# Kernel optimization log

Hardware: AMD Instinct MI355X
Metric: run time of the kernel (lower is better)

The kernel has to match this reference:

```python
import jax, jax.numpy as jnp
import numpy as np

N_NODES = 50000
N_EDGES = 800000
IN_CH = 128
HID = 128


def _linear_params(key, fan_in, fan_out):
    kw, kb = jax.random.split(key)
    bound = 1.0 / np.sqrt(fan_in)
    W = jax.random.uniform(kw, (fan_in, fan_out), jnp.float32, -bound, bound)
    b = jax.random.uniform(kb, (fan_out,), jnp.float32, -bound, bound)
    return W, b


def setup_inputs() -> dict:
    key = jax.random.key(0)
    ks = jax.random.split(key, 11)
    x = jax.random.normal(ks[0], (N_NODES, IN_CH), jnp.float32)
    guidance_features = jax.random.normal(ks[1], (N_NODES, HID), jnp.float32)
    edge_index = jax.random.randint(ks[2], (2, N_EDGES), 0, N_NODES, jnp.int64)
    node_W, node_b = _linear_params(ks[3], IN_CH, HID)
    nbr_W, nbr_b = _linear_params(ks[4], IN_CH, HID)
    gud_W, gud_b = _linear_params(ks[5], HID, HID)
    enc_W, enc_b = _linear_params(ks[6], 3 * HID, HID)
    vp_W1, vp_b1 = _linear_params(ks[7], HID, HID // 2)
    vp_W2, vp_b2 = _linear_params(ks[8], HID // 2, 1)
    pol_W1, pol_b1 = _linear_params(ks[9], HID, HID)
    pol_W2, pol_b2 = _linear_params(ks[10], HID, 1)
    return dict(x=x, edge_index=edge_index, guidance_features=guidance_features,
                node_W=node_W, node_b=node_b, nbr_W=nbr_W, nbr_b=nbr_b,
                gud_W=gud_W, gud_b=gud_b, enc_W=enc_W, enc_b=enc_b,
                vp_W1=vp_W1, vp_b1=vp_b1, vp_W2=vp_W2, vp_b2=vp_b2,
                pol_W1=pol_W1, pol_b1=pol_b1, pol_W2=pol_W2, pol_b2=pol_b2)


def reference(x, edge_index, guidance_features,
              node_W, node_b, nbr_W, nbr_b, gud_W, gud_b,
              enc_W, enc_b, vp_W1, vp_b1, vp_W2, vp_b2,
              pol_W1, pol_b1, pol_W2, pol_b2):
    row, col = edge_index[0], edge_index[1]
    # Edge-wise gathers feeding three linear transforms -> [E, 3*HID] state
    node_feat = x[row] @ node_W + node_b            # [E, HID]
    nbr_feat = x[col] @ nbr_W + nbr_b               # [E, HID]
    gud_feat = guidance_features[col] @ gud_W + gud_b  # [E, HID]
    state = jnp.concatenate([node_feat, nbr_feat, gud_feat], axis=1)
    # state_encoder (eval mode: dropout = identity)
    enc = jax.nn.relu(state @ enc_W + enc_b)        # [E, HID]
    # value_predictor
    value_preds = jax.nn.relu(enc @ vp_W1 + vp_b1) @ vp_W2 + vp_b2  # [E, 1]
    # policy_net
    action_probs = jax.nn.sigmoid(
        jax.nn.relu(enc @ pol_W1 + pol_b1) @ pol_W2 + pol_b2)      # [E, 1]
    actions = (action_probs > 0.5).astype(x.dtype)  # eval-mode actions
    value_loss = jnp.zeros((), x.dtype)             # eval mode, labels=None
    return value_preds, action_probs, actions, value_loss
```

## Files before the change

kernel.cpp:

```cpp
#include <hip/hip_runtime.h>
#include <math.h>

#define N_NODES 50000
#define N_EDGES 800000

typedef __attribute__((ext_vector_type(8))) short short8_t;
typedef __attribute__((ext_vector_type(4))) float float4_t;

union U8 { short8_t v; unsigned short u[8]; };

__device__ __forceinline__ unsigned short bf16_rn(float f) {
    unsigned u = __float_as_uint(f);
    u += 0x7fffu + ((u >> 16) & 1u);
    return (unsigned short)(u >> 16);
}
__device__ __forceinline__ float bf2f(unsigned short h) {
    return __uint_as_float((unsigned)h << 16);
}
__device__ __forceinline__ void split3(float f, unsigned short& s0,
                                       unsigned short& s1, unsigned short& s2) {
    s0 = bf16_rn(f);  float r = f - bf2f(s0);
    s1 = bf16_rn(r);  r -= bf2f(s1);
    s2 = bf16_rn(r);
}


__global__ __launch_bounds__(256) void prep_kernel(
    const float* __restrict__ node_W, const float* __restrict__ node_b,
    const float* __restrict__ nbr_W,  const float* __restrict__ nbr_b,
    const float* __restrict__ gud_W,  const float* __restrict__ gud_b,
    const float* __restrict__ enc_W,  const float* __restrict__ enc_b,
    const float* __restrict__ vp_W1,  const float* __restrict__ vp_b1,
    const float* __restrict__ vp_W2,  const float* __restrict__ pol_W1,
    const float* __restrict__ pol_b1, const float* __restrict__ pol_W2,
    unsigned short* __restrict__ BTn0, unsigned short* __restrict__ BTn1,
    unsigned short* __restrict__ BTn2,
    unsigned short* __restrict__ BTg0, unsigned short* __restrict__ BTg1,
    unsigned short* __restrict__ BTg2,
    unsigned short* __restrict__ BTw0, unsigned short* __restrict__ BTw1,
    unsigned short* __restrict__ BTw2,
    float* __restrict__ cb, float* __restrict__ b1c, float* __restrict__ W2c,
    int* __restrict__ flags)
{
    const int k = blockIdx.x;
    const int j = threadIdx.x;
    if (j < 128) {
        float a = 0.f, b = 0.f;
        #pragma unroll 4
        for (int m = 0; m < 128; ++m) {
            a = fmaf(node_W[k * 128 + m], enc_W[m * 128 + j], a);
            b = fmaf(gud_W [k * 128 + m], enc_W[(256 + m) * 128 + j], b);
        }
        size_t i1 = (size_t)j * 128 + k;
        split3(a, BTn0[i1], BTn1[i1], BTn2[i1]);
        split3(b, BTg0[i1], BTg1[i1], BTg2[i1]);
    } else {
        const int n = j - 128;
        float a = 0.f;
        #pragma unroll 4
        for (int m = 0; m < 128; ++m)
            a = fmaf(nbr_W[k * 128 + m], enc_W[(128 + m) * 128 + n], a);
        size_t i2 = (size_t)(128 + n) * 128 + k;
        split3(a, BTn0[i2], BTn1[i2], BTn2[i2]);
    }
    if (j < 192) {
        float wv = (j < 64) ? vp_W1[k * 64 + j] : pol_W1[k * 128 + (j - 64)];
        size_t iw = (size_t)j * 128 + k;
        split3(wv, BTw0[iw], BTw1[iw], BTw2[iw]);
    }
    if (k == 0) {
        if (j < 128) {
            float cc = enc_b[j];
            for (int m = 0; m < 128; ++m) {
                cc = fmaf(node_b[m], enc_W[m * 128 + j], cc);
                cc = fmaf(nbr_b [m], enc_W[(128 + m) * 128 + j], cc);
                cc = fmaf(gud_b [m], enc_W[(256 + m) * 128 + j], cc);
            }
            cb[j] = cc;
        }
        if (j < 192) {
            b1c[j] = (j < 64) ? vp_b1[j] : pol_b1[j - 64];
            W2c[j] = (j < 64) ? vp_W2[j] : pol_W2[j - 64];
        }
        if (j < 64) {
            const int l = j, li = l & 15, lq = l >> 4;
            U8 A, B;
            #pragma unroll
            for (int u = 0; u < 8; ++u) { A.u[u] = 0; B.u[u] = 0; }
            if (lq == 0) {
                A.u[0] = bf16_rn((float)(li + 1));
                A.u[1] = bf16_rn(1.0f);
                B.u[0] = bf16_rn(1.0f);
                B.u[1] = bf16_rn((float)(100 * (li + 1)));
            }
            float4_t d = (float4_t){0.f, 0.f, 0.f, 0.f};
            d = __builtin_amdgcn_mfma_f32_16x16x32_bf16(A.v, B.v, d, 0, 0, 0);
            if (l == 17) {
                flags[0] = (fabsf(d[2] - 702.f) < 1.0f) ? 1 : 0;
            }
        }
    }
}

__global__ __launch_bounds__(256, 2) void node_kernel(
    const float* __restrict__ x, const float* __restrict__ g,
    const unsigned short* __restrict__ BTn0, const unsigned short* __restrict__ BTn1,
    const unsigned short* __restrict__ BTn2,
    const unsigned short* __restrict__ BTg0, const unsigned short* __restrict__ BTg1,
    const unsigned short* __restrict__ BTg2,
    const float* __restrict__ cb, const int* __restrict__ flags,
    float* __restrict__ P, float* __restrict__ Q)
{
    const int t = threadIdx.x;
    const int w = t >> 6, lane = t & 63;
    const int i16 = lane & 15, q = lane >> 4;
    const int base = blockIdx.x * 64;
    const bool qhalf = (w >= 2);
    const int nt0 = w * 4;
    const int kcmax = qhalf ? 8 : 4;
    const int swap = flags[0];

    float4_t acc[4][4];
    #pragma unroll
    for (int mt = 0; mt < 4; ++mt)
        #pragma unroll
        for (int nt = 0; nt < 4; ++nt) acc[mt][nt] = (float4_t){0.f, 0.f, 0.f, 0.f};

    for (int kc = 0; kc < kcmax; ++kc) {
        short8_t b0[4], b1v[4], b2v[4];
        #pragma unroll
        for (int nt = 0; nt < 4; ++nt) {
            if (kc < 4) {
                size_t roff = ((size_t)((nt0 + nt) * 16 + i16)) * 128 + kc * 32 + q * 8;
                b0[nt]  = *(const short8_t*)(BTn0 + roff);
                b1v[nt] = *(const short8_t*)(BTn1 + roff);
                b2v[nt] = *(const short8_t*)(BTn2 + roff);
            } else {
                size_t roff = ((size_t)((nt0 + nt - 8) * 16 + i16)) * 128 + (kc - 4) * 32 + q * 8;
                b0[nt]  = *(const short8_t*)(BTg0 + roff);
                b1v[nt] = *(const short8_t*)(BTg1 + roff);
                b2v[nt] = *(const short8_t*)(BTg2 + roff);
            }
        }
        #pragma unroll
        for (int mt = 0; mt < 4; ++mt) {
            int node = base + mt * 16 + i16; if (node > N_NODES - 1) node = N_NODES - 1;
            const float* src = (kc < 4)
                ? (x + (size_t)node * 128 + kc * 32 + q * 8)
                : (g + (size_t)node * 128 + (kc - 4) * 32 + q * 8);
            float4 v0 = *(const float4*)(src);
            float4 v1 = *(const float4*)(src + 4);
            float e[8] = {v0.x, v0.y, v0.z, v0.w, v1.x, v1.y, v1.z, v1.w};
            U8 a0, a1, a2;
            #pragma unroll
            for (int u = 0; u < 8; ++u) split3(e[u], a0.u[u], a1.u[u], a2.u[u]);
            #pragma unroll
            for (int nt = 0; nt < 4; ++nt) {
                float4_t c = acc[mt][nt];
                c = __builtin_amdgcn_mfma_f32_16x16x32_bf16(a0.v, b0[nt],  c, 0, 0, 0);
                c = __builtin_amdgcn_mfma_f32_16x16x32_bf16(a0.v, b1v[nt], c, 0, 0, 0);
                c = __builtin_amdgcn_mfma_f32_16x16x32_bf16(a1.v, b0[nt],  c, 0, 0, 0);
                c = __builtin_amdgcn_mfma_f32_16x16x32_bf16(a0.v, b2v[nt], c, 0, 0, 0);
                c = __builtin_amdgcn_mfma_f32_16x16x32_bf16(a1.v, b1v[nt], c, 0, 0, 0);
                c = __builtin_amdgcn_mfma_f32_16x16x32_bf16(a2.v, b0[nt],  c, 0, 0, 0);
                acc[mt][nt] = c;
            }
        }
    }

    if (!swap) {
        #pragma unroll
        for (int mt = 0; mt < 4; ++mt)
            #pragma unroll
            for (int nt = 0; nt < 4; ++nt) {
                int chan = (nt0 + nt) * 16 + i16;
                float bias = qhalf ? 0.f : cb[chan];
                #pragma unroll
                for (int r = 0; r < 4; ++r) {
                    int node = base + mt * 16 + q * 4 + r;
                    if (node < N_NODES) {
                        if (!qhalf) P[(size_t)node * 128 + chan] = acc[mt][nt][r] + bias;
                        else        Q[(size_t)node * 128 + (chan - 128)] = acc[mt][nt][r];
                    }
                }
            }
    } else {
        #pragma unroll
        for (int mt = 0; mt < 4; ++mt) {
            int node = base + mt * 16 + i16;
            if (node < N_NODES) {
                #pragma unroll
                for (int nt = 0; nt < 4; ++nt) {
                    int chanb = (nt0 + nt) * 16 + q * 4;
                    float4 vv;
                    vv.x = acc[mt][nt][0] + (!qhalf ? cb[chanb + 0] : 0.f);
                    vv.y = acc[mt][nt][1] + (!qhalf ? cb[chanb + 1] : 0.f);
                    vv.z = acc[mt][nt][2] + (!qhalf ? cb[chanb + 2] : 0.f);
                    vv.w = acc[mt][nt][3] + (!qhalf ? cb[chanb + 3] : 0.f);
                    if (!qhalf) *(float4*)(P + (size_t)node * 128 + chanb) = vv;
                    else        *(float4*)(Q + (size_t)node * 128 + chanb - 128) = vv;
                }
            }
        }
    }
}

__global__ __launch_bounds__(256, 2) void edge_kernel(
    const int* __restrict__ ei,
    const float* __restrict__ P, const float* __restrict__ Q,
    const unsigned short* __restrict__ BTw0, const unsigned short* __restrict__ BTw1,
    const unsigned short* __restrict__ BTw2,
    const float* __restrict__ b1c, const float* __restrict__ W2c,
    const float* __restrict__ vp_b2, const float* __restrict__ pol_b2,
    const int* __restrict__ flags,
    float* __restrict__ out)
{
    __shared__ unsigned short enc0[4 * 128 * 8];
    __shared__ unsigned short enc1[4 * 128 * 8];
    __shared__ unsigned short enc2[4 * 128 * 8];
    __shared__ int rows_s[128], cols_s[128];
    __shared__ float vpart[512], ppart[512];

    const int t = threadIdx.x;
    const int w = t >> 6, lane = t & 63;
    const int i16 = lane & 15, q = lane >> 4;
    const int e0 = blockIdx.x * 128;
    const int ntg0 = w * 3;
    const int el = t & 127, hh = t >> 7;
    const int swap = flags[0];

    if (t < 128) rows_s[t] = ei[e0 + t];
    else         cols_s[t - 128] = ei[N_EDGES + e0 + (t - 128)];

    float4_t acc[8][3];
    #pragma unroll
    for (int mt = 0; mt < 8; ++mt)
        #pragma unroll
        for (int nt = 0; nt < 3; ++nt) acc[mt][nt] = (float4_t){0.f, 0.f, 0.f, 0.f};

    for (int kc = 0; kc < 4; ++kc) {
        __syncthreads();
        {
            const float* Pp = P + (size_t)rows_s[el] * 128 + kc * 32 + hh * 16;
            const float* Qp = Q + (size_t)cols_s[el] * 128 + kc * 32 + hh * 16;
            U8 g0[2], g1[2], g2[2];
            #pragma unroll
            for (int i = 0; i < 4; ++i) {
                float4 pv = *(const float4*)(Pp + i * 4);
                float4 qv = *(const float4*)(Qp + i * 4);
                float ev[4] = {fmaxf(pv.x + qv.x, 0.f), fmaxf(pv.y + qv.y, 0.f),
                               fmaxf(pv.z + qv.z, 0.f), fmaxf(pv.w + qv.w, 0.f)};
                #pragma unroll
                for (int u = 0; u < 4; ++u) {
                    int idx = i * 4 + u;
                    split3(ev[u], g0[idx >> 3].u[idx & 7], g1[idx >> 3].u[idx & 7],
                           g2[idx >> 3].u[idx & 7]);
                }
            }
            #pragma unroll
            for (int hb = 0; hb < 2; ++hb) {
                size_t off = ((size_t)(2 * hh + hb) * 128 + el) * 8;
                *(short8_t*)(enc0 + off) = g0[hb].v;
                *(short8_t*)(enc1 + off) = g1[hb].v;
                *(short8_t*)(enc2 + off) = g2[hb].v;
            }
        }
        __syncthreads();
        short8_t b0[3], b1f[3], b2f[3];
        #pragma unroll
        for (int ntl = 0; ntl < 3; ++ntl) {
            size_t roff = ((size_t)((ntg0 + ntl) * 16 + i16)) * 128 + kc * 32 + q * 8;
            b0[ntl]  = *(const short8_t*)(BTw0 + roff);
            b1f[ntl] = *(const short8_t*)(BTw1 + roff);
            b2f[ntl] = *(const short8_t*)(BTw2 + roff);
        }
        #pragma unroll
        for (int mt = 0; mt < 8; ++mt) {
            size_t aoff = ((size_t)q * 128 + mt * 16 + i16) * 8;
            short8_t a0 = *(const short8_t*)(enc0 + aoff);
            short8_t a1 = *(const short8_t*)(enc1 + aoff);
            short8_t a2 = *(const short8_t*)(enc2 + aoff);
            #pragma unroll
            for (int ntl = 0; ntl < 3; ++ntl) {
                float4_t c = acc[mt][ntl];
                c = __builtin_amdgcn_mfma_f32_16x16x32_bf16(a0, b0[ntl],  c, 0, 0, 0);
                c = __builtin_amdgcn_mfma_f32_16x16x32_bf16(a0, b1f[ntl], c, 0, 0, 0);
                c = __builtin_amdgcn_mfma_f32_16x16x32_bf16(a1, b0[ntl],  c, 0, 0, 0);
                c = __builtin_amdgcn_mfma_f32_16x16x32_bf16(a0, b2f[ntl], c, 0, 0, 0);
                c = __builtin_amdgcn_mfma_f32_16x16x32_bf16(a1, b1f[ntl], c, 0, 0, 0);
                c = __builtin_amdgcn_mfma_f32_16x16x32_bf16(a2, b0[ntl],  c, 0, 0, 0);
                acc[mt][ntl] = c;
            }
        }
    }

    if (!swap) {
        #pragma unroll
        for (int mt = 0; mt < 8; ++mt) {
            float vs[4] = {0.f, 0.f, 0.f, 0.f}, ps[4] = {0.f, 0.f, 0.f, 0.f};
            #pragma unroll
            for (int ntl = 0; ntl < 3; ++ntl) {
                int ntg = ntg0 + ntl;
                int n = ntg * 16 + i16;
                float b1s = b1c[n], w2s = W2c[n];
                bool isv = (ntg < 4);
                #pragma unroll
                for (int r = 0; r < 4; ++r) {
                    float hv = fmaxf(acc[mt][ntl][r] + b1s, 0.f) * w2s;
                    if (isv) vs[r] += hv; else ps[r] += hv;
                }
            }
            #pragma unroll
            for (int off = 1; off < 16; off <<= 1)
                #pragma unroll
                for (int r = 0; r < 4; ++r) {
                    vs[r] += __shfl_xor(vs[r], off, 64);
                    ps[r] += __shfl_xor(ps[r], off, 64);
                }
            if (i16 == 0)
                #pragma unroll
                for (int r = 0; r < 4; ++r) {
                    int eidx = mt * 16 + q * 4 + r;
                    vpart[w * 128 + eidx] = vs[r];
                    ppart[w * 128 + eidx] = ps[r];
                }
        }
    } else {
        #pragma unroll
        for (int mt = 0; mt < 8; ++mt) {
            float v = 0.f, p = 0.f;
            #pragma unroll
            for (int ntl = 0; ntl < 3; ++ntl) {
                int ntg = ntg0 + ntl;
                bool isv = (ntg < 4);
                #pragma unroll
                for (int r = 0; r < 4; ++r) {
                    int n = ntg * 16 + q * 4 + r;
                    float hv = fmaxf(acc[mt][ntl][r] + b1c[n], 0.f) * W2c[n];
                    if (isv) v += hv; else p += hv;
                }
            }
            v += __shfl_xor(v, 16, 64); v += __shfl_xor(v, 32, 64);
            p += __shfl_xor(p, 16, 64); p += __shfl_xor(p, 32, 64);
            if (q == 0) {
                int eidx = mt * 16 + i16;
                vpart[w * 128 + eidx] = v;
                ppart[w * 128 + eidx] = p;
            }
        }
    }
    __syncthreads();
    if (t < 128) {
        float v  = vpart[t] + vpart[128 + t] + vpart[256 + t] + vpart[384 + t] + vp_b2[0];
        float pl = ppart[t] + ppart[128 + t] + ppart[256 + t] + ppart[384 + t] + pol_b2[0];
        float prob = 1.0f / (1.0f + expf(-pl));
        int e = e0 + t;
        out[e] = v;
        out[N_EDGES + e] = prob;
        out[2 * N_EDGES + e] = (prob > 0.5f) ? 1.0f : 0.0f;
    }
    if (blockIdx.x == 0 && t == 0) out[3 * N_EDGES] = 0.0f;
}

extern "C" void kernel_launch(void* const* d_in, const int* in_sizes, int n_in,
                              void* d_out, int out_size, void* d_ws, size_t ws_size,
                              hipStream_t stream) {
    const float* x      = (const float*)d_in[0];
    const int*   ei     = (const int*)  d_in[1];
    const float* gf     = (const float*)d_in[2];
    const float* node_W = (const float*)d_in[3];
    const float* node_b = (const float*)d_in[4];
    const float* nbr_W  = (const float*)d_in[5];
    const float* nbr_b  = (const float*)d_in[6];
    const float* gud_W  = (const float*)d_in[7];
    const float* gud_b  = (const float*)d_in[8];
    const float* enc_W  = (const float*)d_in[9];
    const float* enc_b  = (const float*)d_in[10];
    const float* vp_W1  = (const float*)d_in[11];
    const float* vp_b1  = (const float*)d_in[12];
    const float* vp_W2  = (const float*)d_in[13];
    const float* vp_b2  = (const float*)d_in[14];
    const float* pol_W1 = (const float*)d_in[15];
    const float* pol_b1 = (const float*)d_in[16];
    const float* pol_W2 = (const float*)d_in[17];
    const float* pol_b2 = (const float*)d_in[18];
    float* out = (float*)d_out;

    unsigned char* wsb = (unsigned char*)d_ws;
    unsigned short* BTn0 = (unsigned short*)(wsb + 0);
    unsigned short* BTn1 = (unsigned short*)(wsb + 65536);
    unsigned short* BTn2 = (unsigned short*)(wsb + 131072);
    unsigned short* BTg0 = (unsigned short*)(wsb + 196608);
    unsigned short* BTg1 = (unsigned short*)(wsb + 229376);
    unsigned short* BTg2 = (unsigned short*)(wsb + 262144);
    unsigned short* BTw0 = (unsigned short*)(wsb + 294912);
    unsigned short* BTw1 = (unsigned short*)(wsb + 344064);
    unsigned short* BTw2 = (unsigned short*)(wsb + 393216);
    float* cb   = (float*)(wsb + 442368);
    float* b1c  = (float*)(wsb + 442880);
    float* W2c  = (float*)(wsb + 443648);
    int*   flags= (int*)  (wsb + 444416);
    float* Pd   = (float*)(wsb + 444480);
    float* Qd   = Pd + (size_t)N_NODES * 128;

    prep_kernel<<<dim3(128), dim3(256), 0, stream>>>(
        node_W, node_b, nbr_W, nbr_b, gud_W, gud_b, enc_W, enc_b,
        vp_W1, vp_b1, vp_W2, pol_W1, pol_b1, pol_W2,
        BTn0, BTn1, BTn2, BTg0, BTg1, BTg2, BTw0, BTw1, BTw2,
        cb, b1c, W2c, flags);

    node_kernel<<<dim3((N_NODES + 63) / 64), dim3(256), 0, stream>>>(
        x, gf, BTn0, BTn1, BTn2, BTg0, BTg1, BTg2, cb, flags, Pd, Qd);

    edge_kernel<<<dim3(N_EDGES / 128), dim3(256), 0, stream>>>(
        ei, Pd, Qd, BTw0, BTw1, BTw2, b1c, W2c, vp_b2, pol_b2, flags, out);
}
```

Baseline: 588.8 us.

## Prefetch gathered rows into registers and stage split operands through shared memory

```diff
diff --git a/kernel.cpp b/kernel.cpp
--- a/kernel.cpp
+++ b/kernel.cpp
@@ -22,6 +22,16 @@
     s0 = bf16_rn(f);  float r = f - bf2f(s0);
     s1 = bf16_rn(r);  r -= bf2f(s1);
     s2 = bf16_rn(r);
+}
+__device__ __forceinline__ void split3t(float f, unsigned short& s0,
+                                        unsigned short& s1, unsigned short& s2) {
+    unsigned u = __float_as_uint(f);
+    s0 = (unsigned short)(u >> 16);
+    float r = f - bf2f(s0);
+    unsigned v = __float_as_uint(r);
+    s1 = (unsigned short)(v >> 16);
+    float r2 = r - bf2f(s1);
+    s2 = bf16_rn(r2);
 }
 
 
@@ -102,7 +112,7 @@
     }
 }
 
-__global__ __launch_bounds__(256, 2) void node_kernel(
+__global__ __launch_bounds__(256, 3) void node_kernel(
     const float* __restrict__ x, const float* __restrict__ g,
     const unsigned short* __restrict__ BTn0, const unsigned short* __restrict__ BTn1,
     const unsigned short* __restrict__ BTn2,
@@ -111,14 +121,18 @@
     const float* __restrict__ cb, const int* __restrict__ flags,
     float* __restrict__ P, float* __restrict__ Q)
 {
+    __shared__ unsigned short a0s[4 * 64 * 8];
+    __shared__ unsigned short a1s[4 * 64 * 8];
+    __shared__ unsigned short a2s[4 * 64 * 8];
     const int t = threadIdx.x;
     const int w = t >> 6, lane = t & 63;
     const int i16 = lane & 15, q = lane >> 4;
     const int base = blockIdx.x * 64;
-    const bool qhalf = (w >= 2);
-    const int nt0 = w * 4;
-    const int kcmax = qhalf ? 8 : 4;
     const int swap = flags[0];
+    const int el = t >> 2, hh = t & 3;
+    int nodeL = base + el; if (nodeL > N_NODES - 1) nodeL = N_NODES - 1;
+    const float* xrow = x + (size_t)nodeL * 128 + hh * 8;
+    const float* grow = g + (size_t)nodeL * 128 + hh * 8;
 
     float4_t acc[4][4];
     #pragma unroll
@@ -126,44 +140,85 @@
         #pragma unroll
         for (int nt = 0; nt < 4; ++nt) acc[mt][nt] = (float4_t){0.f, 0.f, 0.f, 0.f};
 
-    for (int kc = 0; kc < kcmax; ++kc) {
-        short8_t b0[4], b1v[4], b2v[4];
-        #pragma unroll
-        for (int nt = 0; nt < 4; ++nt) {
-            if (kc < 4) {
-                size_t roff = ((size_t)((nt0 + nt) * 16 + i16)) * 128 + kc * 32 + q * 8;
-                b0[nt]  = *(const short8_t*)(BTn0 + roff);
-                b1v[nt] = *(const short8_t*)(BTn1 + roff);
-                b2v[nt] = *(const short8_t*)(BTn2 + roff);
-            } else {
-                size_t roff = ((size_t)((nt0 + nt - 8) * 16 + i16)) * 128 + (kc - 4) * 32 + q * 8;
-                b0[nt]  = *(const short8_t*)(BTg0 + roff);
-                b1v[nt] = *(const short8_t*)(BTg1 + roff);
-                b2v[nt] = *(const short8_t*)(BTg2 + roff);
-            }
-        }
-        #pragma unroll
-        for (int mt = 0; mt < 4; ++mt) {
-            int node = base + mt * 16 + i16; if (node > N_NODES - 1) node = N_NODES - 1;
-            const float* src = (kc < 4)
-                ? (x + (size_t)node * 128 + kc * 32 + q * 8)
-                : (g + (size_t)node * 128 + (kc - 4) * 32 + q * 8);
-            float4 v0 = *(const float4*)(src);
-            float4 v1 = *(const float4*)(src + 4);
-            float e[8] = {v0.x, v0.y, v0.z, v0.w, v1.x, v1.y, v1.z, v1.w};
-            U8 a0, a1, a2;
-            #pragma unroll
-            for (int u = 0; u < 8; ++u) split3(e[u], a0.u[u], a1.u[u], a2.u[u]);
-            #pragma unroll
-            for (int nt = 0; nt < 4; ++nt) {
-                float4_t c = acc[mt][nt];
-                c = __builtin_amdgcn_mfma_f32_16x16x32_bf16(a0.v, b0[nt],  c, 0, 0, 0);
-                c = __builtin_amdgcn_mfma_f32_16x16x32_bf16(a0.v, b1v[nt], c, 0, 0, 0);
-                c = __builtin_amdgcn_mfma_f32_16x16x32_bf16(a1.v, b0[nt],  c, 0, 0, 0);
-                c = __builtin_amdgcn_mfma_f32_16x16x32_bf16(a0.v, b2v[nt], c, 0, 0, 0);
-                c = __builtin_amdgcn_mfma_f32_16x16x32_bf16(a1.v, b1v[nt], c, 0, 0, 0);
-                c = __builtin_amdgcn_mfma_f32_16x16x32_bf16(a2.v, b0[nt],  c, 0, 0, 0);
-                acc[mt][nt] = c;
+    float4 pv0 = *(const float4*)(xrow);
+    float4 pv1 = *(const float4*)(xrow + 4);
+
+    for (int kc = 0; kc < 8; ++kc) {
+        U8 s0, s1, s2;
+        {
+            float e[8] = {pv0.x, pv0.y, pv0.z, pv0.w, pv1.x, pv1.y, pv1.z, pv1.w};
+            #pragma unroll
+            for (int u = 0; u < 8; ++u) split3t(e[u], s0.u[u], s1.u[u], s2.u[u]);
+        }
+        __syncthreads();
+        {
+            size_t off = ((size_t)hh * 64 + el) * 8;
+            *(short8_t*)(a0s + off) = s0.v;
+            *(short8_t*)(a1s + off) = s1.v;
+            *(short8_t*)(a2s + off) = s2.v;
+        }
+        __syncthreads();
+        if (kc < 7) {
+            const float* nsrc = (kc + 1 < 4) ? (xrow + (kc + 1) * 32)
+                                             : (grow + (kc + 1 - 4) * 32);
+            pv0 = *(const float4*)(nsrc);
+            pv1 = *(const float4*)(nsrc + 4);
+        }
+        if (kc < 4) {
+            short8_t b0[4], b1v[4], b2v[4];
+            #pragma unroll
+            for (int ntl = 0; ntl < 4; ++ntl) {
+                int ntg = w + ntl * 4;
+                size_t roff = ((size_t)(ntg * 16 + i16)) * 128 + kc * 32 + q * 8;
+                b0[ntl]  = *(const short8_t*)(BTn0 + roff);
+                b1v[ntl] = *(const short8_t*)(BTn1 + roff);
+                b2v[ntl] = *(const short8_t*)(BTn2 + roff);
+            }
+            #pragma unroll
+            for (int mt = 0; mt < 4; ++mt) {
+                size_t aoff = ((size_t)q * 64 + mt * 16 + i16) * 8;
+                short8_t a0 = *(const short8_t*)(a0s + aoff);
+                short8_t a1 = *(const short8_t*)(a1s + aoff);
+                short8_t a2 = *(const short8_t*)(a2s + aoff);
+                #pragma unroll
+                for (int ntl = 0; ntl < 4; ++ntl) {
+                    float4_t c = acc[mt][ntl];
+                    c = __builtin_amdgcn_mfma_f32_16x16x32_bf16(a0, b0[ntl],  c, 0, 0, 0);
+                    c = __builtin_amdgcn_mfma_f32_16x16x32_bf16(a0, b1v[ntl], c, 0, 0, 0);
+                    c = __builtin_amdgcn_mfma_f32_16x16x32_bf16(a1, b0[ntl],  c, 0, 0, 0);
+                    c = __builtin_amdgcn_mfma_f32_16x16x32_bf16(a0, b2v[ntl], c, 0, 0, 0);
+                    c = __builtin_amdgcn_mfma_f32_16x16x32_bf16(a1, b1v[ntl], c, 0, 0, 0);
+                    c = __builtin_amdgcn_mfma_f32_16x16x32_bf16(a2, b0[ntl],  c, 0, 0, 0);
+                    acc[mt][ntl] = c;
+                }
+            }
+        } else {
+            short8_t b0[2], b1v[2], b2v[2];
+            #pragma unroll
+            for (int ntl = 0; ntl < 2; ++ntl) {
+                int ntg = w + (ntl + 2) * 4;
+                size_t roff = ((size_t)((ntg - 8) * 16 + i16)) * 128 + (kc - 4) * 32 + q * 8;
+                b0[ntl]  = *(const short8_t*)(BTg0 + roff);
+                b1v[ntl] = *(const short8_t*)(BTg1 + roff);
+                b2v[ntl] = *(const short8_t*)(BTg2 + roff);
+            }
+            #pragma unroll
+            for (int mt = 0; mt < 4; ++mt) {
+                size_t aoff = ((size_t)q * 64 + mt * 16 + i16) * 8;
+                short8_t a0 = *(const short8_t*)(a0s + aoff);
+                short8_t a1 = *(const short8_t*)(a1s + aoff);
+                short8_t a2 = *(const short8_t*)(a2s + aoff);
+                #pragma unroll
+                for (int ntl = 0; ntl < 2; ++ntl) {
+                    float4_t c = acc[mt][ntl + 2];
+                    c = __builtin_amdgcn_mfma_f32_16x16x32_bf16(a0, b0[ntl],  c, 0, 0, 0);
+                    c = __builtin_amdgcn_mfma_f32_16x16x32_bf16(a0, b1v[ntl], c, 0, 0, 0);
+                    c = __builtin_amdgcn_mfma_f32_16x16x32_bf16(a1, b0[ntl],  c, 0, 0, 0);
+                    c = __builtin_amdgcn_mfma_f32_16x16x32_bf16(a0, b2v[ntl], c, 0, 0, 0);
+                    c = __builtin_amdgcn_mfma_f32_16x16x32_bf16(a1, b1v[ntl], c, 0, 0, 0);
+                    c = __builtin_amdgcn_mfma_f32_16x16x32_bf16(a2, b0[ntl],  c, 0, 0, 0);
+                    acc[mt][ntl + 2] = c;
+                }
             }
         }
     }
@@ -172,15 +227,17 @@
         #pragma unroll
         for (int mt = 0; mt < 4; ++mt)
             #pragma unroll
-            for (int nt = 0; nt < 4; ++nt) {
-                int chan = (nt0 + nt) * 16 + i16;
-                float bias = qhalf ? 0.f : cb[chan];
+            for (int ntl = 0; ntl < 4; ++ntl) {
+                int ntg = w + ntl * 4;
+                int chan = ntg * 16 + i16;
+                bool isP = (ntg < 8);
+                float bias = isP ? cb[chan] : 0.f;
                 #pragma unroll
                 for (int r = 0; r < 4; ++r) {
                     int node = base + mt * 16 + q * 4 + r;
                     if (node < N_NODES) {
-                        if (!qhalf) P[(size_t)node * 128 + chan] = acc[mt][nt][r] + bias;
-                        else        Q[(size_t)node * 128 + (chan - 128)] = acc[mt][nt][r];
+                        if (isP) P[(size_t)node * 128 + chan] = acc[mt][ntl][r] + bias;
+                        else     Q[(size_t)node * 128 + (chan - 128)] = acc[mt][ntl][r];
                     }
                 }
             }
@@ -190,15 +247,17 @@
             int node = base + mt * 16 + i16;
             if (node < N_NODES) {
                 #pragma unroll
-                for (int nt = 0; nt < 4; ++nt) {
-                    int chanb = (nt0 + nt) * 16 + q * 4;
+                for (int ntl = 0; ntl < 4; ++ntl) {
+                    int ntg = w + ntl * 4;
+                    int chanb = ntg * 16 + q * 4;
+                    bool isP = (ntg < 8);
                     float4 vv;
-                    vv.x = acc[mt][nt][0] + (!qhalf ? cb[chanb + 0] : 0.f);
-                    vv.y = acc[mt][nt][1] + (!qhalf ? cb[chanb + 1] : 0.f);
-                    vv.z = acc[mt][nt][2] + (!qhalf ? cb[chanb + 2] : 0.f);
-                    vv.w = acc[mt][nt][3] + (!qhalf ? cb[chanb + 3] : 0.f);
-                    if (!qhalf) *(float4*)(P + (size_t)node * 128 + chanb) = vv;
-                    else        *(float4*)(Q + (size_t)node * 128 + chanb - 128) = vv;
+                    vv.x = acc[mt][ntl][0] + (isP ? cb[chanb + 0] : 0.f);
+                    vv.y = acc[mt][ntl][1] + (isP ? cb[chanb + 1] : 0.f);
+                    vv.z = acc[mt][ntl][2] + (isP ? cb[chanb + 2] : 0.f);
+                    vv.w = acc[mt][ntl][3] + (isP ? cb[chanb + 3] : 0.f);
+                    if (isP) *(float4*)(P + (size_t)node * 128 + chanb) = vv;
+                    else     *(float4*)(Q + (size_t)node * 128 + chanb - 128) = vv;
                 }
             }
         }
@@ -218,7 +277,6 @@
     __shared__ unsigned short enc0[4 * 128 * 8];
     __shared__ unsigned short enc1[4 * 128 * 8];
     __shared__ unsigned short enc2[4 * 128 * 8];
-    __shared__ int rows_s[128], cols_s[128];
     __shared__ float vpart[512], ppart[512];
 
     const int t = threadIdx.x;
@@ -226,11 +284,13 @@
     const int i16 = lane & 15, q = lane >> 4;
     const int e0 = blockIdx.x * 128;
     const int ntg0 = w * 3;
-    const int el = t & 127, hh = t >> 7;
+    const int el = t >> 1, hh = t & 1;
     const int swap = flags[0];
 
-    if (t < 128) rows_s[t] = ei[e0 + t];
-    else         cols_s[t - 128] = ei[N_EDGES + e0 + (t - 128)];
+    const int rowI = ei[e0 + el];
+    const int colI = ei[N_EDGES + e0 + el];
+    const float* Pp = P + (size_t)rowI * 128 + hh * 16;
+    const float* Qp = Q + (size_t)colI * 128 + hh * 16;
 
     float4_t acc[8][3];
     #pragma unroll
@@ -238,34 +298,42 @@
         #pragma unroll
         for (int nt = 0; nt < 3; ++nt) acc[mt][nt] = (float4_t){0.f, 0.f, 0.f, 0.f};
 
+    float4 pv[4], qv[4];
+    #pragma unroll
+    for (int i = 0; i < 4; ++i) {
+        pv[i] = *(const float4*)(Pp + i * 4);
+        qv[i] = *(const float4*)(Qp + i * 4);
+    }
+
     for (int kc = 0; kc < 4; ++kc) {
+        U8 g0[2], g1[2], g2[2];
+        #pragma unroll
+        for (int i = 0; i < 4; ++i) {
+            float ev[4] = {fmaxf(pv[i].x + qv[i].x, 0.f), fmaxf(pv[i].y + qv[i].y, 0.f),
+                           fmaxf(pv[i].z + qv[i].z, 0.f), fmaxf(pv[i].w + qv[i].w, 0.f)};
+            #pragma unroll
+            for (int u = 0; u < 4; ++u) {
+                int idx = i * 4 + u;
+                split3t(ev[u], g0[idx >> 3].u[idx & 7], g1[idx >> 3].u[idx & 7],
+                        g2[idx >> 3].u[idx & 7]);
+            }
+        }
         __syncthreads();
-        {
-            const float* Pp = P + (size_t)rows_s[el] * 128 + kc * 32 + hh * 16;
-            const float* Qp = Q + (size_t)cols_s[el] * 128 + kc * 32 + hh * 16;
-            U8 g0[2], g1[2], g2[2];
+        #pragma unroll
+        for (int hb = 0; hb < 2; ++hb) {
+            size_t off = ((size_t)(2 * hh + hb) * 128 + el) * 8;
+            *(short8_t*)(enc0 + off) = g0[hb].v;
+            *(short8_t*)(enc1 + off) = g1[hb].v;
+            *(short8_t*)(enc2 + off) = g2[hb].v;
+        }
+        __syncthreads();
+        if (kc < 3) {
             #pragma unroll
             for (int i = 0; i < 4; ++i) {
-                float4 pv = *(const float4*)(Pp + i * 4);
-                float4 qv = *(const float4*)(Qp + i * 4);
-                float ev[4] = {fmaxf(pv.x + qv.x, 0.f), fmaxf(pv.y + qv.y, 0.f),
-                               fmaxf(pv.z + qv.z, 0.f), fmaxf(pv.w + qv.w, 0.f)};
-                #pragma unroll
-                for (int u = 0; u < 4; ++u) {
-                    int idx = i * 4 + u;
-                    split3(ev[u], g0[idx >> 3].u[idx & 7], g1[idx >> 3].u[idx & 7],
-                           g2[idx >> 3].u[idx & 7]);
-                }
-            }
-            #pragma unroll
-            for (int hb = 0; hb < 2; ++hb) {
-                size_t off = ((size_t)(2 * hh + hb) * 128 + el) * 8;
-                *(short8_t*)(enc0 + off) = g0[hb].v;
-                *(short8_t*)(enc1 + off) = g1[hb].v;
-                *(short8_t*)(enc2 + off) = g2[hb].v;
-            }
-        }
-        __syncthreads();
+                pv[i] = *(const float4*)(Pp + (kc + 1) * 32 + i * 4);
+                qv[i] = *(const float4*)(Qp + (kc + 1) * 32 + i * 4);
+            }
+        }
         short8_t b0[3], b1f[3], b2f[3];
         #pragma unroll
         for (int ntl = 0; ntl < 3; ++ntl) {
```

New measurement: 518.9 us. 11.9% less time.
